# Optimization experiments

Hardware: AMD Instinct MI355X
Metric: run time of the kernel (lower is better)

## Reference

```python
import jax, jax.numpy as jnp
import numpy as np

D_MODEL = 512
N_HEAD = 8
D_HEAD = D_MODEL // N_HEAD


def _linear(x, W, b):
    return x @ W + b


def setup_inputs() -> dict:
    key = jax.random.key(0)
    ks = jax.random.split(key, 20)
    B, N, D = 8, 1024, D_MODEL
    H = D // 2
    s = 1.0 / np.sqrt(D)
    s2 = 1.0 / np.sqrt(H)
    inp = {
        'query': jax.random.normal(ks[0], (B, N, D), jnp.float32),
        'key_in': jax.random.normal(ks[1], (B, N, D), jnp.float32),
        'value': jax.random.normal(ks[2], (B, N, D), jnp.float32),
        'Wq': jax.random.normal(ks[3], (D, D), jnp.float32) * s,
        'bq': jnp.zeros((D,), jnp.float32),
        'Wk': jax.random.normal(ks[4], (D, D), jnp.float32) * s,
        'bk': jnp.zeros((D,), jnp.float32),
        'Wv': jax.random.normal(ks[5], (D, D), jnp.float32) * s,
        'bv': jnp.zeros((D,), jnp.float32),
        'Wo': jax.random.normal(ks[6], (D, D), jnp.float32) * s,
        'bo': jnp.zeros((D,), jnp.float32),
        'Ws1': jax.random.normal(ks[7], (D, H), jnp.float32) * s,
        'bs1': jnp.zeros((H,), jnp.float32),
        'Ws2': jax.random.normal(ks[8], (H, D), jnp.float32) * s2,
        'bs2': jnp.zeros((D,), jnp.float32),
        'Wc1': jax.random.normal(ks[9], (D, H), jnp.float32) * s,
        'bc1': jnp.zeros((H,), jnp.float32),
        'Wc2': jax.random.normal(ks[10], (H, D), jnp.float32) * s2,
        'bc2': jnp.zeros((D,), jnp.float32),
    }
    return inp


def reference(query, key_in, value, Wq, bq, Wk, bk, Wv, bv, Wo, bo,
              Ws1, bs1, Ws2, bs2, Wc1, bc1, Wc2, bc2):
    B, N, D = query.shape
    H, Dh = N_HEAD, D_HEAD

    def split_heads(x):  # [b, n, h*d] -> [b, h, n, d]
        return x.reshape(B, N, H, Dh).transpose(0, 2, 1, 3)

    q = split_heads(_linear(query, Wq, bq))
    k = split_heads(_linear(key_in, Wk, bk))
    vv = _linear(value, Wv, bv)  # [b, n, d] == rearrange(v,'b h n d->b n (h d)')

    # spatial gating: Linear-ReLU-Linear-Sigmoid on w_v(value)
    sw = jax.nn.sigmoid(_linear(jax.nn.relu(_linear(vv, Ws1, bs1)), Ws2, bs2))
    v_spatial = split_heads(vv * sw)

    # channel gating: MLP on mean-over-seq profile, broadcast back to seq
    prof = value.mean(axis=1, keepdims=True)  # [b, 1, d]
    cw = jax.nn.sigmoid(_linear(jax.nn.relu(_linear(prof, Wc1, bc1)), Wc2, bc2))
    v_channel = split_heads(_linear(value * cw, Wv, bv))

    v_dual = v_spatial + v_channel

    scores = jnp.einsum('bhqd,bhkd->bhqk', q, k) / np.sqrt(Dh).astype(np.float32)
    attn = jax.nn.softmax(scores, axis=-1)
    out = jnp.einsum('bhqk,bhkd->bhqd', attn, v_dual)
    out = out.transpose(0, 2, 1, 3).reshape(B, N, D)
    return _linear(out, Wo, bo)  # dropout is identity in eval mode
```

## Files before the change

kernel.cpp:

```cpp
#include <hip/hip_runtime.h>

typedef unsigned short u16t;
typedef __bf16  bf8   __attribute__((ext_vector_type(8)));
typedef float   f32x4 __attribute__((ext_vector_type(4)));
typedef unsigned short us4 __attribute__((ext_vector_type(4)));

#define DEV __device__ __forceinline__

DEV float bf2f(u16t u) { union { unsigned u; float f; } x; x.u = ((unsigned)u) << 16; return x.f; }
DEV u16t  f2bf(float f) {
    union { float f; unsigned u; } x; x.f = f;
    unsigned r = x.u + 0x7FFFu + ((x.u >> 16) & 1u);
    return (u16t)(r >> 16);
}
DEV uint4 pack8(const float* v) {
    uint4 r;
    r.x = (unsigned)f2bf(v[0]) | ((unsigned)f2bf(v[1]) << 16);
    r.y = (unsigned)f2bf(v[2]) | ((unsigned)f2bf(v[3]) << 16);
    r.z = (unsigned)f2bf(v[4]) | ((unsigned)f2bf(v[5]) << 16);
    r.w = (unsigned)f2bf(v[6]) | ((unsigned)f2bf(v[7]) << 16);
    return r;
}
DEV void gll16(const void* g, void* l) {
    __builtin_amdgcn_global_load_lds(
        (const __attribute__((address_space(1))) unsigned*)g,
        (__attribute__((address_space(3))) unsigned*)l, 16, 0, 0);
}

#define DMODEL 512
#define SEQ    1024
#define NBATCH 8

__global__ __launch_bounds__(256) void fill_sentinel(float* out, int n)
{
    int i = blockIdx.x * 256 + threadIdx.x;
    if (i < n) out[i] = 100.f;
}

__global__ __launch_bounds__(256) void cvt3(const float* q, const float* k,
                                            const float* v,
                                            u16t* Qb, u16t* Kb, u16t* Vb)
{
    int y = blockIdx.y;
    const float* s = (y == 0) ? q : (y == 1) ? k : v;
    u16t*        d = (y == 0) ? Qb : (y == 1) ? Kb : Vb;
    size_t i = ((size_t)blockIdx.x * 256 + threadIdx.x) * 8;
    float4 a = *(const float4*)(s + i), b = *(const float4*)(s + i + 4);
    float o[8] = {a.x, a.y, a.z, a.w, b.x, b.y, b.z, b.w};
    *(uint4*)&d[i] = pack8(o);
}

__global__ __launch_bounds__(256) void transpose6(
    const float* s0, const float* s1, const float* s2, const float* s3,
    const float* s4, const float* s5,
    u16t* d0, u16t* d1, u16t* d2, u16t* d3, u16t* d4, u16t* d5)
{
    int z = blockIdx.z;
    const float* S; u16t* D; int R, C;
    switch (z) {
        case 0: S = s0; D = d0; R = 512; C = 512; break;
        case 1: S = s1; D = d1; R = 512; C = 512; break;
        case 2: S = s2; D = d2; R = 512; C = 512; break;
        case 3: S = s3; D = d3; R = 512; C = 512; break;
        case 4: S = s4; D = d4; R = 512; C = 256; break;
        default:S = s5; D = d5; R = 256; C = 512; break;
    }
    int c0 = blockIdx.x * 32, r0 = blockIdx.y * 32;
    if (c0 >= C || r0 >= R) return;
    __shared__ u16t tile[32][33];
    int tx = threadIdx.x & 31, ty = threadIdx.x >> 5;
#pragma unroll
    for (int p = 0; p < 4; ++p) {
        int r = ty + p * 8;
        tile[r][tx] = f2bf(S[(size_t)(r0 + r) * C + c0 + tx]);
    }
    __syncthreads();
#pragma unroll
    for (int p = 0; p < 4; ++p) {
        int r = ty + p * 8;
        D[(size_t)(c0 + r) * R + r0 + tx] = tile[tx][r];
    }
}

__global__ __launch_bounds__(256) void colmean(const u16t* Vi, float* prof)
{
    int b = blockIdx.y, z = blockIdx.z;
    int d = blockIdx.x * 256 + threadIdx.x;
    const u16t* p = Vi + (size_t)b * SEQ * DMODEL + (size_t)z * 64 * DMODEL + d;
    float s = 0.f;
#pragma unroll 8
    for (int n = 0; n < 64; ++n) s += bf2f(p[(size_t)n * DMODEL]);
    atomicAdd(&prof[b * DMODEL + d], s * (1.f / 1024.f));
}

__global__ __launch_bounds__(256) void cmlp(const float* prof,
                                            const float* Wc1, const float* bc1,
                                            const float* Wc2, const float* bc2,
                                            u16t* cw)
{
    int b = blockIdx.x, t = threadIdx.x;
    __shared__ float pf[512];
    __shared__ float hf[256];
    pf[t]       = prof[b * 512 + t];
    pf[t + 256] = prof[b * 512 + t + 256];
    __syncthreads();
    float s = bc1[t];
    for (int k = 0; k < 512; ++k) s += pf[k] * Wc1[(size_t)k * 256 + t];
    hf[t] = fmaxf(s, 0.f);
    __syncthreads();
#pragma unroll
    for (int o = 0; o < 2; ++o) {
        int d = t + o * 256;
        float s2 = bc2[d];
        for (int k = 0; k < 256; ++k) s2 += hf[k] * Wc2[(size_t)k * 512 + d];
        cw[b * 512 + d] = f2bf(1.f / (1.f + __expf(-s2)));
    }
}

__global__ __launch_bounds__(256) void scale_wv(const u16t* WvT, const u16t* cw,
                                                u16t* WvTs)
{
    int b = blockIdx.y;
    int idx = blockIdx.x * 2048 + threadIdx.x * 8;
    int k = idx & 511;
    uint4 wv = *(const uint4*)&WvT[idx];
    uint4 cu = *(const uint4*)&cw[b * 512 + k];
    const u16t* wp = (const u16t*)&wv;
    const u16t* cp = (const u16t*)&cu;
    float o[8];
#pragma unroll
    for (int q = 0; q < 8; ++q) o[q] = bf2f(wp[q]) * bf2f(cp[q]);
    *(uint4*)&WvTs[(size_t)b * 262144 + idx] = pack8(o);
}

template<int MINW, int WR, int WC, int WM, int NT>
__global__ __launch_bounds__(256, MINW) void gemmP(
    const u16t* A0, const u16t* A1, const u16t* A2, const u16t* A3,
    const u16t* W0, const u16t* W1, const u16t* W2, const u16t* W3,
    const float* B0, const float* B1, const float* B2, const float* B3,
    void* C0, void* C1, void* C2, void* C3,
    int N, int K, int mode,
    const u16t* VVp, u16t* VdTp,
    int tmask, int outf32, int wbmask)
{
    constexpr int BM = WR * WM * 16;
    constexpr int BN = WC * NT * 16;
    constexpr int PA = BM / 64;
    constexpr int PB = BN / 64;
    constexpr int LPT = PA + PB;

    int z = blockIdx.z;
    const u16t* A  = (z == 0) ? A0 : (z == 1) ? A1 : (z == 2) ? A2 : A3;
    const u16t* W  = (z == 0) ? W0 : (z == 1) ? W1 : (z == 2) ? W2 : W3;
    const float* Bi = (z == 0) ? B0 : (z == 1) ? B1 : (z == 2) ? B2 : B3;
    void*       C  = (z == 0) ? C0 : (z == 1) ? C1 : (z == 2) ? C2 : C3;

    int tstore = (tmask >> z) & 1;

    int tid = threadIdx.x;
    int w = tid >> 6, lane = tid & 63, quad = lane >> 4, l16 = lane & 15;
    int wr = w / WC, wc = w % WC;
    int m0 = blockIdx.x * BM, n0 = blockIdx.y * BN;
    int bb = m0 >> 10;
    if ((wbmask >> z) & 1) W += (size_t)bb * 262144;

    __shared__ __align__(16) u16t As[3][BM * 32];
    __shared__ __align__(16) u16t Bs[3][BN * 32];

    const u16t* srcA[PA];
#pragma unroll
    for (int p = 0; p < PA; ++p) {
        int ci = p * 256 + tid, r = ci >> 2, g = ci & 3;
        srcA[p] = A + (size_t)(m0 + r) * K + (g ^ (r & 3)) * 8;
    }
    const u16t* srcB[PB];
#pragma unroll
    for (int p = 0; p < PB; ++p) {
        int ci = p * 256 + tid, r = ci >> 2, g = ci & 3;
        srcB[p] = W + (size_t)(n0 + r) * K + (g ^ (r & 3)) * 8;
    }

    f32x4 zero = {0.f, 0.f, 0.f, 0.f};
    f32x4 acc[WM][NT];
#pragma unroll
    for (int mi = 0; mi < WM; ++mi)
#pragma unroll
        for (int ni = 0; ni < NT; ++ni) acc[mi][ni] = zero;

    auto stage = [&](int buf, int k0) {
#pragma unroll
        for (int p = 0; p < PA; ++p)
            gll16(srcA[p] + k0, &As[buf][(size_t)(p * 256 + w * 64) * 8]);
#pragma unroll
        for (int p = 0; p < PB; ++p)
            gll16(srcB[p] + k0, &Bs[buf][(size_t)(p * 256 + w * 64) * 8]);
    };
    auto compute = [&](int buf) {
        int sx = l16 & 3;
        bf8 af[WM], bfr[NT];
#pragma unroll
        for (int mi = 0; mi < WM; ++mi)
            af[mi] = *(const bf8*)&As[buf][(wr * WM * 16 + mi * 16 + l16) * 32 + ((quad ^ sx) * 8)];
#pragma unroll
        for (int ni = 0; ni < NT; ++ni)
            bfr[ni] = *(const bf8*)&Bs[buf][(wc * NT * 16 + ni * 16 + l16) * 32 + ((quad ^ sx) * 8)];
#pragma unroll
        for (int mi = 0; mi < WM; ++mi)
#pragma unroll
            for (int ni = 0; ni < NT; ++ni)
                acc[mi][ni] = __builtin_amdgcn_mfma_f32_16x16x32_bf16(af[mi], bfr[ni], acc[mi][ni], 0, 0, 0);
    };

    int nt = K >> 5;
    stage(0, 0);
    stage(1, 32);
    for (int t = 0; t < nt; ++t) {
        if (t + 1 < nt)
            asm volatile("s_waitcnt vmcnt(%0) lgkmcnt(0)" :: "n"(LPT) : "memory");
        else
            asm volatile("s_waitcnt vmcnt(0) lgkmcnt(0)" ::: "memory");
        __builtin_amdgcn_s_barrier();
        __builtin_amdgcn_sched_barrier(0);
        compute(t % 3);
        if (t + 2 < nt) stage((t + 2) % 3, (t + 2) << 5);
    }

#pragma unroll
    for (int mi = 0; mi < WM; ++mi) {
        int grow0 = m0 + wr * WM * 16 + mi * 16 + quad * 4;
#pragma unroll
        for (int ni = 0; ni < NT; ++ni) {
            int gcol = n0 + wc * NT * 16 + ni * 16 + l16;
            float bias = Bi[gcol];
            if (mode == 2) {
                int h = gcol >> 6, dh = gcol & 63;
                int b_ = grow0 >> 10, n_ = grow0 & 1023;
                size_t tbase = (size_t)((b_ * 8 + h) * 64 + dh) * 1024 + n_;
                us4 vc = *(const us4*)&VdTp[tbase];
                us4 pk;
#pragma unroll
                for (int r = 0; r < 4; ++r) {
                    float s = acc[mi][ni][r] + bias;
                    float sw = 1.f / (1.f + __expf(-s));
                    float vvv = bf2f(VVp[(size_t)(grow0 + r) * DMODEL + gcol]);
                    pk[r] = f2bf(vvv * sw + bf2f(vc[r]));
                }
                *(us4*)&VdTp[tbase] = pk;
            } else if (tstore) {
                int h = gcol >> 6, dh = gcol & 63;
                int b_ = grow0 >> 10, n_ = grow0 & 1023;
                us4 pk;
#pragma unroll
                for (int r = 0; r < 4; ++r) pk[r] = f2bf(acc[mi][ni][r] + bias);
                *(us4*)&((u16t*)C)[(size_t)((b_ * 8 + h) * 64 + dh) * 1024 + n_] = pk;
            } else if (outf32) {
#pragma unroll
                for (int r = 0; r < 4; ++r)
                    ((float*)C)[(size_t)(grow0 + r) * N + gcol] = acc[mi][ni][r] + bias;
            } else {
#pragma unroll
                for (int r = 0; r < 4; ++r) {
                    float v = acc[mi][ni][r] + bias;
                    if (mode == 1) v = fmaxf(v, 0.f);
                    ((u16t*)C)[(size_t)(grow0 + r) * N + gcol] = f2bf(v);
                }
            }
        }
    }
}

__global__ __launch_bounds__(256, 3) void attn(const u16t* Q, const u16t* Km,
                                               const u16t* VdT, u16t* Oa)
{
    __shared__ __align__(16) u16t Qs[64 * 64];
    __shared__ __align__(16) u16t Ks[2][64 * 64];
    __shared__ __align__(16) u16t Vs[2][64 * 64];
    __shared__ __align__(16) u16t Ps[64 * 64];

    int qt = blockIdx.x, bh = blockIdx.y;
    int b = bh >> 3, h = bh & 7;
    int tid = threadIdx.x;
    int w = tid >> 6, lane = tid & 63, quad = lane >> 4, l16 = lane & 15;
    int l7 = l16 & 7;

    const u16t* Qp = Q   + ((size_t)(b * SEQ + qt * 64)) * DMODEL + h * 64;
    const u16t* Kp = Km  + ((size_t)(b * SEQ)) * DMODEL + h * 64;
    const u16t* Vp = VdT + ((size_t)(b * 8 + h)) * 64 * SEQ;

    auto stageKV = [&](int buf, int kt2) {
#pragma unroll
        for (int p = 0; p < 2; ++p) {
            int ci = p * 256 + tid;
            int r = ci >> 3, g = ci & 7;
            int gs = (g ^ (r & 7)) * 8;
            gll16(&Kp[(size_t)(kt2 * 64 + r) * DMODEL + gs], &Ks[buf][(size_t)(p * 256 + w * 64) * 8]);
            gll16(&Vp[(size_t)r * SEQ + kt2 * 64 + gs],      &Vs[buf][(size_t)(p * 256 + w * 64) * 8]);
        }
    };

#pragma unroll
    for (int p = 0; p < 2; ++p) {
        int ci = p * 256 + tid;
        int r = ci >> 3, g = ci & 7;
        int gs = (g ^ (r & 7)) * 8;
        gll16(&Qp[(size_t)r * DMODEL + gs], &Qs[(size_t)(p * 256 + w * 64) * 8]);
    }
    stageKV(0, 0);

    f32x4 zero = {0.f, 0.f, 0.f, 0.f};
    f32x4 oacc[4];
    float l_run[4];
#pragma unroll
    for (int r = 0; r < 4; ++r) { l_run[r] = 0.f; oacc[r] = zero; }

    for (int kt = 0; kt < 16; ++kt) {
        int buf = kt & 1;
        asm volatile("s_waitcnt vmcnt(0) lgkmcnt(0)" ::: "memory");
        __builtin_amdgcn_s_barrier();
        __builtin_amdgcn_sched_barrier(0);

        f32x4 sacc[4];
#pragma unroll
        for (int j = 0; j < 4; ++j) sacc[j] = zero;
#pragma unroll
        for (int ks = 0; ks < 2; ++ks) {
            int sG = ((ks * 4 + quad) ^ l7) * 8;
            bf8 aq = *(const bf8*)&Qs[(w * 16 + l16) * 64 + sG];
            bf8 bk[4];
#pragma unroll
            for (int j = 0; j < 4; ++j)
                bk[j] = *(const bf8*)&Ks[buf][(j * 16 + l16) * 64 + sG];
#pragma unroll
            for (int j = 0; j < 4; ++j)
                sacc[j] = __builtin_amdgcn_mfma_f32_16x16x32_bf16(aq, bk[j], sacc[j], 0, 0, 0);
        }

        if (kt + 1 < 16) stageKV(buf ^ 1, kt + 1);

#pragma unroll
        for (int r4 = 0; r4 < 4; ++r4) {
            float rsum = 0.f;
            int prow = w * 16 + quad * 4 + r4;
            int pr7 = prow & 7;
#pragma unroll
            for (int j = 0; j < 4; ++j) {
                float p = __expf(fmaf(sacc[j][r4], 0.125f, -4.f));
                rsum += p;
                int G = j * 2 + (l16 >> 3);
                Ps[prow * 64 + ((G ^ pr7) * 8) + l7] = f2bf(p);
            }
#pragma unroll
            for (int d = 1; d < 16; d <<= 1) rsum += __shfl_xor(rsum, d);
            l_run[r4] += rsum;
        }

#pragma unroll
        for (int kk = 0; kk < 2; ++kk) {
            int sG = ((kk * 4 + quad) ^ l7) * 8;
            bf8 ap = *(const bf8*)&Ps[(w * 16 + l16) * 64 + sG];
            bf8 bvf[4];
#pragma unroll
            for (int j = 0; j < 4; ++j)
                bvf[j] = *(const bf8*)&Vs[buf][(j * 16 + l16) * 64 + sG];
#pragma unroll
            for (int j = 0; j < 4; ++j)
                oacc[j] = __builtin_amdgcn_mfma_f32_16x16x32_bf16(ap, bvf[j], oacc[j], 0, 0, 0);
        }
    }

#pragma unroll
    for (int j = 0; j < 4; ++j) {
#pragma unroll
        for (int r4 = 0; r4 < 4; ++r4) {
            int rq = qt * 64 + w * 16 + quad * 4 + r4;
            float v = oacc[j][r4] / l_run[r4];
            Oa[((size_t)(b * SEQ + rq)) * DMODEL + h * 64 + j * 16 + l16] = f2bf(v);
        }
    }
}

extern "C" void kernel_launch(void* const* d_in, const int* in_sizes, int n_in,
                              void* d_out, int out_size, void* d_ws, size_t ws_size,
                              hipStream_t stream)
{
    const float* query  = (const float*)d_in[0];
    const float* key_in = (const float*)d_in[1];
    const float* value  = (const float*)d_in[2];
    const float* Wq  = (const float*)d_in[3];  const float* bq  = (const float*)d_in[4];
    const float* Wk  = (const float*)d_in[5];  const float* bk  = (const float*)d_in[6];
    const float* Wv  = (const float*)d_in[7];  const float* bv  = (const float*)d_in[8];
    const float* Wo  = (const float*)d_in[9];  const float* bo  = (const float*)d_in[10];
    const float* Ws1 = (const float*)d_in[11]; const float* bs1 = (const float*)d_in[12];
    const float* Ws2 = (const float*)d_in[13]; const float* bs2 = (const float*)d_in[14];
    const float* Wc1 = (const float*)d_in[15]; const float* bc1 = (const float*)d_in[16];
    const float* Wc2 = (const float*)d_in[17]; const float* bc2 = (const float*)d_in[18];
    float* out = (float*)d_out;

    u16t* ws = (u16t*)d_ws;
    u16t* WqT  = ws + 0;
    u16t* WkT  = ws + 262144;
    u16t* WvT  = ws + 524288;
    u16t* WoT  = ws + 786432;
    u16t* Ws1T = ws + 1048576;
    u16t* Ws2T = ws + 1179648;
    u16t* WvTs = ws + 1310720;
    u16t* Vi   = ws + 3407872;
    u16t* Qm   = ws + 7602176;
    u16t* Kmm  = ws + 11796480;
    u16t* VV   = ws + 15990784;
    u16t* VdT  = ws + 20185088;
    u16t* cw   = ws + 24379392;
    float* prof = (float*)(ws + 24383488);
    u16t* Qbf  = ws + 24391680;
    u16t* Kbf  = ws + 28585984;
    u16t* H1 = Vi;
    u16t* Oa = VV;

    const size_t NEED_BYTES = 32780288ull * 2ull;
    if (ws_size < NEED_BYTES) {
        fill_sentinel<<<(out_size + 255) / 256, 256, 0, stream>>>(out, out_size);
        return;
    }

    hipMemsetAsync((void*)prof, 0, NBATCH * DMODEL * sizeof(float), stream);

    cvt3<<<dim3(2048, 3), 256, 0, stream>>>(query, key_in, value, Qbf, Kbf, Vi);
    transpose6<<<dim3(16, 16, 6), 256, 0, stream>>>(Wq, Wk, Wv, Wo, Ws1, Ws2,
                                                    WqT, WkT, WvT, WoT, Ws1T, Ws2T);
    colmean<<<dim3(2, 8, 16), 256, 0, stream>>>(Vi, prof);
    cmlp<<<8, 256, 0, stream>>>(prof, Wc1, bc1, Wc2, bc2, cw);
    scale_wv<<<dim3(128, 8), 256, 0, stream>>>(WvT, cw, WvTs);

    gemmP<2, 2, 2, 4, 8><<<dim3(64, 2, 4), 256, 0, stream>>>(
        Qbf, Kbf, Vi, Vi,
        WqT, WkT, WvT, WvTs,
        bq, bk, bv, bv,
        Qm, Kmm, VV, VdT,
        512, 512, 0, nullptr, VdT,
        0x8, 0, 0x8);

    gemmP<4, 2, 2, 2, 2><<<dim3(128, 4, 1), 256, 0, stream>>>(
        VV, VV, VV, VV, Ws1T, Ws1T, Ws1T, Ws1T, bs1, bs1, bs1, bs1,
        H1, H1, H1, H1, 256, 512, 1, nullptr, nullptr, 0, 0, 0);

    gemmP<4, 2, 2, 2, 2><<<dim3(128, 8, 1), 256, 0, stream>>>(
        H1, H1, H1, H1, Ws2T, Ws2T, Ws2T, Ws2T, bs2, bs2, bs2, bs2,
        Qm, Qm, Qm, Qm,
        512, 256, 2, VV, VdT, 0, 0, 0);

    attn<<<dim3(16, 64), 256, 0, stream>>>(Qm, Kmm, VdT, Oa);

    gemmP<4, 2, 2, 2, 2><<<dim3(128, 8, 1), 256, 0, stream>>>(
        Oa, Oa, Oa, Oa, WoT, WoT, WoT, WoT, bo, bo, bo, bo,
        out, out, out, out, 512, 512, 0, nullptr, nullptr,
        0, 1, 0);
}
```

Before: 274.4 us.

## Keep attention probabilities in registers via transposed QK MFMA and bpermute

The QK^T MFMA operands are swapped so each lane holds scores for a single query row. The probabilities are packed to bf16 and redistributed into the PV A-operand layout with ds_bpermute, which removes the Ps shared-memory buffer and its store/load round trip. Freeing that LDS allows the launch-bounds occupancy hint to go from 3 to 4 blocks, and the row-sum reduction needs fewer shuffles. In exchange it adds bpermute traffic and selects, and the lane-to-row mapping for the final normalisation must stay correct.

Measured after the change: 262.1 us. 1.05x faster.

```diff
diff --git a/kernel.cpp b/kernel.cpp
--- a/kernel.cpp
+++ b/kernel.cpp
@@ -269,19 +269,21 @@
     }
 }
 
-__global__ __launch_bounds__(256, 3) void attn(const u16t* Q, const u16t* Km,
+__global__ __launch_bounds__(256, 4) void attn(const u16t* Q, const u16t* Km,
                                                const u16t* VdT, u16t* Oa)
 {
     __shared__ __align__(16) u16t Qs[64 * 64];
     __shared__ __align__(16) u16t Ks[2][64 * 64];
     __shared__ __align__(16) u16t Vs[2][64 * 64];
-    __shared__ __align__(16) u16t Ps[64 * 64];
 
     int qt = blockIdx.x, bh = blockIdx.y;
     int b = bh >> 3, h = bh & 7;
     int tid = threadIdx.x;
     int w = tid >> 6, lane = tid & 63, quad = lane >> 4, l16 = lane & 15;
     int l7 = l16 & 7;
+    int ht = quad >> 1;
+    int sA = ((quad & 1) * 32 + l16) * 4;
+    int sB = sA + 64;
 
     const u16t* Qp = Q   + ((size_t)(b * SEQ + qt * 64)) * DMODEL + h * 64;
     const u16t* Kp = Km  + ((size_t)(b * SEQ)) * DMODEL + h * 64;
@@ -309,9 +311,9 @@
 
     f32x4 zero = {0.f, 0.f, 0.f, 0.f};
     f32x4 oacc[4];
-    float l_run[4];
-#pragma unroll
-    for (int r = 0; r < 4; ++r) { l_run[r] = 0.f; oacc[r] = zero; }
+#pragma unroll
+    for (int r = 0; r < 4; ++r) oacc[r] = zero;
+    float l_run = 0.f;
 
     for (int kt = 0; kt < 16; ++kt) {
         int buf = kt & 1;
@@ -332,48 +334,69 @@
                 bk[j] = *(const bf8*)&Ks[buf][(j * 16 + l16) * 64 + sG];
 #pragma unroll
             for (int j = 0; j < 4; ++j)
-                sacc[j] = __builtin_amdgcn_mfma_f32_16x16x32_bf16(aq, bk[j], sacc[j], 0, 0, 0);
+                sacc[j] = __builtin_amdgcn_mfma_f32_16x16x32_bf16(bk[j], aq, sacc[j], 0, 0, 0);
         }
 
         if (kt + 1 < 16) stageKV(buf ^ 1, kt + 1);
 
-#pragma unroll
-        for (int r4 = 0; r4 < 4; ++r4) {
-            float rsum = 0.f;
-            int prow = w * 16 + quad * 4 + r4;
-            int pr7 = prow & 7;
-#pragma unroll
-            for (int j = 0; j < 4; ++j) {
-                float p = __expf(fmaf(sacc[j][r4], 0.125f, -4.f));
-                rsum += p;
-                int G = j * 2 + (l16 >> 3);
-                Ps[prow * 64 + ((G ^ pr7) * 8) + l7] = f2bf(p);
+        float p[4][4];
+        float rsum = 0.f;
+#pragma unroll
+        for (int j = 0; j < 4; ++j)
+#pragma unroll
+            for (int r = 0; r < 4; ++r) {
+                p[j][r] = __expf(fmaf(sacc[j][r], 0.125f, -4.f));
+                rsum += p[j][r];
             }
-#pragma unroll
-            for (int d = 1; d < 16; d <<= 1) rsum += __shfl_xor(rsum, d);
-            l_run[r4] += rsum;
-        }
-
-#pragma unroll
-        for (int kk = 0; kk < 2; ++kk) {
-            int sG = ((kk * 4 + quad) ^ l7) * 8;
-            bf8 ap = *(const bf8*)&Ps[(w * 16 + l16) * 64 + sG];
+        rsum += __shfl_xor(rsum, 16);
+        rsum += __shfl_xor(rsum, 32);
+        l_run += rsum;
+
+        unsigned pks[8];
+#pragma unroll
+        for (int j = 0; j < 4; ++j)
+#pragma unroll
+            for (int c = 0; c < 2; ++c) {
+                union { __bf16 h[2]; unsigned u; } pk;
+                pk.h[0] = (__bf16)p[j][2 * c];
+                pk.h[1] = (__bf16)p[j][2 * c + 1];
+                pks[2 * j + c] = pk.u;
+            }
+
+#pragma unroll
+        for (int ks = 0; ks < 2; ++ks) {
+            int rA[4], rB[4];
+#pragma unroll
+            for (int c = 0; c < 4; ++c) {
+                rA[c] = __builtin_amdgcn_ds_bpermute(sA, (int)pks[ks * 4 + c]);
+                rB[c] = __builtin_amdgcn_ds_bpermute(sB, (int)pks[ks * 4 + c]);
+            }
+            union { int d[4]; bf8 v; } apu;
+            apu.d[0] = ht ? rA[2] : rA[0];
+            apu.d[1] = ht ? rA[3] : rA[1];
+            apu.d[2] = ht ? rB[2] : rB[0];
+            apu.d[3] = ht ? rB[3] : rB[1];
+            int sG = ((ks * 4 + quad) ^ l7) * 8;
             bf8 bvf[4];
 #pragma unroll
             for (int j = 0; j < 4; ++j)
                 bvf[j] = *(const bf8*)&Vs[buf][(j * 16 + l16) * 64 + sG];
 #pragma unroll
             for (int j = 0; j < 4; ++j)
-                oacc[j] = __builtin_amdgcn_mfma_f32_16x16x32_bf16(ap, bvf[j], oacc[j], 0, 0, 0);
+                oacc[j] = __builtin_amdgcn_mfma_f32_16x16x32_bf16(apu.v, bvf[j], oacc[j], 0, 0, 0);
         }
     }
 
+    float lr[4];
+#pragma unroll
+    for (int r4 = 0; r4 < 4; ++r4)
+        lr[r4] = __shfl(l_run, (quad << 4) | (quad * 4 + r4));
 #pragma unroll
     for (int j = 0; j < 4; ++j) {
 #pragma unroll
         for (int r4 = 0; r4 < 4; ++r4) {
             int rq = qt * 64 + w * 16 + quad * 4 + r4;
-            float v = oacc[j][r4] / l_run[r4];
+            float v = oacc[j][r4] / lr[r4];
             Oa[((size_t)(b * SEQ + rq)) * DMODEL + h * 64 + j * 16 + l16] = f2bf(v);
         }
     }
```
